# Performance work log

Measured on AMD Instinct MI355X. Metric: run time of the kernel, lower is better.

## Reference

```python
import jax, jax.numpy as jnp
import numpy as np

EPS = 1e-5  # BatchNorm eps

def gcn_conv(x, src, dst, deg, dinv, W, b):
    # PyG GCNConv: out = D^{-1/2}(A+I)D^{-1/2} X W + b
    N = x.shape[0]
    xw = x @ W                               # [N, F_out]
    norm = dinv[src] * dinv[dst]             # [E]
    agg = jax.ops.segment_sum(xw[src] * norm[:, None], dst, num_segments=N)
    agg = agg + xw * (1.0 / deg)[:, None]    # self-loop term: deg^-1/2 * deg^-1/2
    return agg + b

def bn(x, g, b, m, v):
    # inference-mode BatchNorm1d over features
    return (x - m) * jax.lax.rsqrt(v + EPS) * g + b

def setup_inputs() -> dict:
    key = jax.random.key(0)
    N, E, F_in, C = 100000, 1600000, 128, 16
    dims = [F_in, 64, 128, 64, 32, C]
    ks = jax.random.split(key, 64)
    inp = {}
    inp["x"] = jax.random.normal(ks[0], (N, F_in), dtype=jnp.float32)
    inp["edge_index"] = jax.random.randint(ks[1], (2, E), 0, N, dtype=jnp.int32)
    ki = 2
    for l in range(5):
        fi, fo = dims[l], dims[l + 1]
        scale = 1.0 / np.sqrt(fi)
        inp[f"w{l+1}"] = jax.random.normal(ks[ki], (fi, fo), dtype=jnp.float32) * scale; ki += 1
        inp[f"b{l+1}"] = jnp.zeros((fo,), dtype=jnp.float32)
    for l in range(4):  # BN params for layers 1..4
        fo = dims[l + 1]
        inp[f"g{l+1}"] = jnp.ones((fo,), dtype=jnp.float32)
        inp[f"be{l+1}"] = jnp.zeros((fo,), dtype=jnp.float32)
        inp[f"m{l+1}"] = jax.random.normal(ks[ki], (fo,), dtype=jnp.float32) * 0.1; ki += 1
        inp[f"v{l+1}"] = jax.random.uniform(ks[ki], (fo,), dtype=jnp.float32, minval=0.5, maxval=1.5); ki += 1
    return inp

def reference(x, edge_index,
              w1, b1, w2, b2, w3, b3, w4, b4, w5, b5,
              g1, be1, m1, v1, g2, be2, m2, v2,
              g3, be3, m3, v3, g4, be4, m4, v4):
    N = x.shape[0]
    src, dst = edge_index[0], edge_index[1]
    deg = jax.ops.segment_sum(jnp.ones(src.shape[0], x.dtype), dst, num_segments=N) + 1.0
    dinv = jax.lax.rsqrt(deg)
    h = jax.nn.relu(bn(gcn_conv(x, src, dst, deg, dinv, w1, b1), g1, be1, m1, v1))
    h = jax.nn.relu(bn(gcn_conv(h, src, dst, deg, dinv, w2, b2), g2, be2, m2, v2))
    h = jax.nn.relu(bn(gcn_conv(h, src, dst, deg, dinv, w3, b3), g3, be3, m3, v3))
    h = jax.nn.relu(bn(gcn_conv(h, src, dst, deg, dinv, w4, b4), g4, be4, m4, v4))
    return gcn_conv(h, src, dst, deg, dinv, w5, b5)
```

## Files before the change

kernel.cpp:

```cpp
#include <hip/hip_runtime.h>
#include <hip/hip_fp16.h>

#define BEPS 1e-5f
static constexpr int TPB = 256;
static constexpr int G_SC = 512;
static constexpr int BK_SHIFT = 8;
static constexpr int BK_NODES = 256;
static constexpr int KMAX = 512;
static constexpr int BK_SLACK = 2048;

union F4H8 { float4 f4; __half2 h2[4]; };

typedef _Float16 half8 __attribute__((ext_vector_type(8)));
typedef float floatx4 __attribute__((ext_vector_type(4)));


__global__ __launch_bounds__(TPB) void k_zero_int(int* __restrict__ p, int n) {
  int i = blockIdx.x * TPB + threadIdx.x;
  if (i < n) p[i] = 0;
}

__global__ __launch_bounds__(TPB) void k_hist(const int* __restrict__ dst,
                                              int* __restrict__ histG,
                                              int* __restrict__ btot,
                                              int E, int K, int chunk) {
  __shared__ int lh[KMAX];
  int g = blockIdx.x, t = threadIdx.x;
  for (int i = t; i < KMAX; i += TPB) lh[i] = 0;
  __syncthreads();
  int e0 = g * chunk, e1 = min(E, e0 + chunk);
  for (int e = e0 + t; e < e1; e += TPB) atomicAdd(&lh[dst[e] >> BK_SHIFT], 1);
  __syncthreads();
  for (int i = t; i < K; i += TPB) {
    histG[i * G_SC + g] = lh[i];
    atomicAdd(&btot[i], lh[i]);
  }
}

__global__ __launch_bounds__(KMAX) void k_bbase(const int* __restrict__ btot,
                                                int* __restrict__ bbase, int K) {
  __shared__ int sh[KMAX];
  int t = threadIdx.x;
  int v = (t < K) ? btot[t] : 0;
  sh[t] = v;
  __syncthreads();
  for (int s = 1; s < KMAX; s <<= 1) {
    int x = sh[t];
    int y = (t >= s) ? sh[t - s] : 0;
    __syncthreads();
    sh[t] = x + y;
    __syncthreads();
  }
  if (t < K) bbase[t] = sh[t] - v;
  if (t == 0) bbase[K] = sh[K - 1];
}

__global__ __launch_bounds__(G_SC) void k_offs(const int* __restrict__ histG,
                                               const int* __restrict__ bbase,
                                               int* __restrict__ offs) {
  __shared__ int sh[G_SC];
  int b = blockIdx.x, t = threadIdx.x;
  int v = histG[b * G_SC + t];
  sh[t] = v;
  __syncthreads();
  for (int s = 1; s < G_SC; s <<= 1) {
    int x = sh[t];
    int y = (t >= s) ? sh[t - s] : 0;
    __syncthreads();
    sh[t] = x + y;
    __syncthreads();
  }
  offs[b * G_SC + t] = bbase[b] + sh[t] - v;
}

__global__ __launch_bounds__(TPB) void k_scatter(const int* __restrict__ src,
                                                 const int* __restrict__ dst,
                                                 const int* __restrict__ offs,
                                                 unsigned int* __restrict__ pairs,
                                                 int E, int K, int chunk) {
  __shared__ int cur[KMAX];
  int g = blockIdx.x, t = threadIdx.x;
  for (int i = t; i < K; i += TPB) cur[i] = offs[i * G_SC + g];
  __syncthreads();
  int e0 = g * chunk, e1 = min(E, e0 + chunk);
  for (int e = e0 + t; e < e1; e += TPB) {
    int d = dst[e];
    int b = d >> BK_SHIFT;
    int pos = atomicAdd(&cur[b], 1);
    pairs[pos] = (unsigned int)src[e] | ((unsigned int)(d & (BK_NODES - 1)) << 20);
  }
}

__global__ __launch_bounds__(TPB) void k_bucket_sort(const unsigned int* __restrict__ pairs,
                                                     const int* __restrict__ bbase,
                                                     int* __restrict__ rowptr,
                                                     int* __restrict__ rowend,
                                                     int* __restrict__ colidx,
                                                     float* __restrict__ dinv,
                                                     int N, int E) {
  __shared__ int cur[BK_NODES];
  __shared__ int sh[BK_NODES];
  int b = blockIdx.x, t = threadIdx.x;
  int base = bbase[b], end = bbase[b + 1];
  int n0 = b << BK_SHIFT;
  int nNodes = min(BK_NODES, N - n0);
  cur[t] = 0;
  __syncthreads();
  for (int e = base + t; e < end; e += TPB) atomicAdd(&cur[pairs[e] >> 20], 1);
  __syncthreads();
  int v = cur[t];
  int pd = (v + 7) & ~7;
  sh[t] = pd;
  __syncthreads();
  for (int s = 1; s < TPB; s <<= 1) {
    int x = sh[t];
    int y = (t >= s) ? sh[t - s] : 0;
    __syncthreads();
    sh[t] = x + y;
    __syncthreads();
  }
  int Bb = (base + b * BK_SLACK + 7) & ~7;
  int start = Bb + (sh[t] - pd);
  if (t < nNodes) {
    rowptr[n0 + t] = start;
    rowend[n0 + t] = start + pd;
    dinv[n0 + t] = rsqrtf((float)(v + 1));
    for (int i = start + v; i < start + pd; ++i) colidx[i] = N;
  }
  __syncthreads();
  cur[t] = start;
  __syncthreads();
  for (int e = base + t; e < end; e += TPB) {
    unsigned int p = pairs[e];
    int pos = atomicAdd(&cur[p >> 20], 1);
    colidx[pos] = (int)(p & 0xFFFFFu);
  }
}

__device__ inline void packone(const float* __restrict__ W, _Float16* __restrict__ Wp,
                               int i, int FO) {
  int j = i & 7, lane = (i >> 3) & 63, tile = i >> 9;
  int nct = FO >> 4, ct = tile % nct, kch = tile / nct;
  int k = kch * 32 + ((lane >> 4) << 3) + j;
  int n = (ct << 4) + (lane & 15);
  Wp[i] = (_Float16)W[k * FO + n];
}

__global__ __launch_bounds__(TPB) void k_packAll(const float* w1, _Float16* p1,
                                                 const float* w2, _Float16* p2,
                                                 const float* w3, _Float16* p3,
                                                 const float* w4, _Float16* p4,
                                                 const float* w5, _Float16* p5,
                                                 __half* bufA, int N) {
  int i = blockIdx.x * TPB + threadIdx.x;
  if (i < 8192) packone(w1, p1, i, 64);
  else if (i < 16384) packone(w2, p2, i - 8192, 128);
  else if (i < 24576) packone(w3, p3, i - 16384, 64);
  else if (i < 26624) packone(w4, p4, i - 24576, 32);
  else if (i < 27136) packone(w5, p5, i - 26624, 16);
  else if (i < 27144) {
    float4 z = {0.f, 0.f, 0.f, 0.f};
    reinterpret_cast<float4*>(bufA + (size_t)64 * N)[i - 27136] = z;
  }
}

template <int FI, int FO, int EPI, bool F32IN>
__global__ __launch_bounds__(TPB) void k_mgemm(const void* __restrict__ hin,
                                               const _Float16* __restrict__ Wp,
                                               const float* __restrict__ dinv,
                                               const float* __restrict__ bias,
                                               const float* __restrict__ g,
                                               const float* __restrict__ be,
                                               const float* __restrict__ m,
                                               const float* __restrict__ v,
                                               __half* __restrict__ out, int N) {
  constexpr int NCT = FO / 16;
  constexpr int NKC = FI / 32;
  __shared__ float4 Wsh[NKC * NCT * 64];
  for (int i = threadIdx.x; i < NKC * NCT * 64; i += TPB)
    Wsh[i] = reinterpret_cast<const float4*>(Wp)[i];
  __syncthreads();

  int lane = threadIdx.x & 63;
  int wv = threadIdx.x >> 6;
  int quad = lane >> 4;
  int rowBase = blockIdx.x * 64 + wv * 16;
  int rA = min(rowBase + (lane & 15), N - 1);

  floatx4 acc[NCT];
#pragma unroll
  for (int ct = 0; ct < NCT; ++ct) acc[ct] = (floatx4){0.f, 0.f, 0.f, 0.f};

#pragma unroll
  for (int kch = 0; kch < NKC; ++kch) {
    half8 a;
    if constexpr (F32IN) {
      const float4* xp = reinterpret_cast<const float4*>(hin);
      size_t idx = ((size_t)rA * FI + kch * 32 + quad * 8) >> 2;
      float4 fa = xp[idx], fb = xp[idx + 1];
      a[0] = (_Float16)fa.x; a[1] = (_Float16)fa.y; a[2] = (_Float16)fa.z; a[3] = (_Float16)fa.w;
      a[4] = (_Float16)fb.x; a[5] = (_Float16)fb.y; a[6] = (_Float16)fb.z; a[7] = (_Float16)fb.w;
    } else {
      union { float4 f4; half8 h8; } ua;
      ua.f4 = reinterpret_cast<const float4*>(hin)[((size_t)rA * FI + kch * 32 + quad * 8) >> 3];
      a = ua.h8;
    }
#pragma unroll
    for (int ct = 0; ct < NCT; ++ct) {
      union { float4 f4; half8 h8; } ub;
      ub.f4 = Wsh[(kch * NCT + ct) * 64 + lane];
      acc[ct] = __builtin_amdgcn_mfma_f32_16x16x32_f16(a, ub.h8, acc[ct], 0, 0, 0);
    }
  }

  int r0 = rowBase + quad * 4;
  if (EPI == 0) {
    float dv[4];
#pragma unroll
    for (int reg = 0; reg < 4; ++reg) dv[reg] = (r0 + reg < N) ? dinv[r0 + reg] : 0.f;
#pragma unroll
    for (int ct = 0; ct < NCT; ++ct) {
      int col = ct * 16 + (lane & 15);
#pragma unroll
      for (int reg = 0; reg < 4; ++reg) {
        int r = r0 + reg;
        out[(size_t)r * FO + col] = __float2half(acc[ct][reg] * dv[reg]);
      }
    }
  } else {
#pragma unroll
    for (int ct = 0; ct < NCT; ++ct) {
      int col = ct * 16 + (lane & 15);
      float sc = g[col] * rsqrtf(v[col] + BEPS);
      float bb = bias[col] - m[col];
      float ee = be[col];
#pragma unroll
      for (int reg = 0; reg < 4; ++reg) {
        int r = r0 + reg;
        out[(size_t)r * FO + col] = __float2half(fmaxf((acc[ct][reg] + bb) * sc + ee, 0.f));
      }
    }
  }
}

template <int F, int MODE, typename TO>
__global__ __launch_bounds__(TPB) void k_agg(const __half* __restrict__ in,
                                             const int* __restrict__ rowptr,
                                             const int* __restrict__ rowend,
                                             const int* __restrict__ colidx,
                                             const float* __restrict__ dinv,
                                             const float* __restrict__ bias,
                                             const float* __restrict__ g,
                                             const float* __restrict__ be,
                                             const float* __restrict__ m,
                                             const float* __restrict__ v,
                                             TO* __restrict__ out, int N) {
  constexpr int V = F / 8;
  constexpr int NPB = TPB / V;
  int node = blockIdx.x * NPB + (int)(threadIdx.x / V);
  int lane = threadIdx.x % V;
  if (node >= N) return;
  const float4* in16 = reinterpret_cast<const float4*>(in);
  const size_t rs = F / 8;
  float acc[8];
  {
    F4H8 u;
    u.f4 = in16[(size_t)node * rs + lane];
#pragma unroll
    for (int i = 0; i < 4; ++i) {
      float2 t2 = __half22float2(u.h2[i]);
      acc[2 * i] = t2.x;
      acc[2 * i + 1] = t2.y;
    }
  }
  int e0 = rowptr[node], e1 = rowend[node];
  int4 c0, c1;
  if (e0 < e1) {
    c0 = *reinterpret_cast<const int4*>(colidx + e0);
    c1 = *reinterpret_cast<const int4*>(colidx + e0 + 4);
  }
  for (int e = e0; e < e1; e += 8) {
    int4 n0, n1;
    int en = e + 8;
    if (en < e1) {
      n0 = *reinterpret_cast<const int4*>(colidx + en);
      n1 = *reinterpret_cast<const int4*>(colidx + en + 4);
    }
    F4H8 u[8];
    u[0].f4 = in16[(size_t)c0.x * rs + lane];
    u[1].f4 = in16[(size_t)c0.y * rs + lane];
    u[2].f4 = in16[(size_t)c0.z * rs + lane];
    u[3].f4 = in16[(size_t)c0.w * rs + lane];
    u[4].f4 = in16[(size_t)c1.x * rs + lane];
    u[5].f4 = in16[(size_t)c1.y * rs + lane];
    u[6].f4 = in16[(size_t)c1.z * rs + lane];
    u[7].f4 = in16[(size_t)c1.w * rs + lane];
#pragma unroll
    for (int q = 0; q < 8; ++q) {
#pragma unroll
      for (int i = 0; i < 4; ++i) {
        float2 t2 = __half22float2(u[q].h2[i]);
        acc[2 * i] += t2.x;
        acc[2 * i + 1] += t2.y;
      }
    }
    c0 = n0; c1 = n1;
  }
  float dv = dinv[node];
#pragma unroll
  for (int i = 0; i < 8; ++i) acc[i] *= dv;
  if (MODE == 0) {
    float4 ba = reinterpret_cast<const float4*>(bias)[lane * 2];
    float4 bb = reinterpret_cast<const float4*>(bias)[lane * 2 + 1];
    acc[0] += ba.x; acc[1] += ba.y; acc[2] += ba.z; acc[3] += ba.w;
    acc[4] += bb.x; acc[5] += bb.y; acc[6] += bb.z; acc[7] += bb.w;
  } else if (MODE == 1 || MODE == 2) {
    const float4* B = reinterpret_cast<const float4*>(bias);
    const float4* G = reinterpret_cast<const float4*>(g);
    const float4* Be = reinterpret_cast<const float4*>(be);
    const float4* M = reinterpret_cast<const float4*>(m);
    const float4* Vv = reinterpret_cast<const float4*>(v);
#pragma unroll
    for (int h = 0; h < 2; ++h) {
      float4 b4 = B[lane * 2 + h], g4 = G[lane * 2 + h], e4 = Be[lane * 2 + h];
      float4 m4 = M[lane * 2 + h], v4 = Vv[lane * 2 + h];
      float* a = acc + 4 * h;
      a[0] = fmaxf((a[0] + b4.x - m4.x) * (g4.x * rsqrtf(v4.x + BEPS)) + e4.x, 0.f);
      a[1] = fmaxf((a[1] + b4.y - m4.y) * (g4.y * rsqrtf(v4.y + BEPS)) + e4.y, 0.f);
      a[2] = fmaxf((a[2] + b4.z - m4.z) * (g4.z * rsqrtf(v4.z + BEPS)) + e4.z, 0.f);
      a[3] = fmaxf((a[3] + b4.w - m4.w) * (g4.w * rsqrtf(v4.w + BEPS)) + e4.w, 0.f);
    }
    if (MODE == 2) {
#pragma unroll
      for (int i = 0; i < 8; ++i) acc[i] *= dv;
    }
  }
  if constexpr (sizeof(TO) == 2) {
    F4H8 u;
#pragma unroll
    for (int i = 0; i < 4; ++i) u.h2[i] = __floats2half2_rn(acc[2 * i], acc[2 * i + 1]);
    reinterpret_cast<float4*>(out)[(size_t)node * rs + lane] = u.f4;
  } else {
    float4 o0 = {acc[0], acc[1], acc[2], acc[3]};
    float4 o1 = {acc[4], acc[5], acc[6], acc[7]};
    float4* op = reinterpret_cast<float4*>((float*)out + (size_t)node * F + lane * 8);
    op[0] = o0;
    op[1] = o1;
  }
}


extern "C" void kernel_launch(void* const* d_in, const int* in_sizes, int n_in,
                              void* d_out, int out_size, void* d_ws, size_t ws_size,
                              hipStream_t stream) {
  const float* x = (const float*)d_in[0];
  const int* ei = (const int*)d_in[1];
  const int N = in_sizes[0] / 128;
  const int E = in_sizes[1] / 2;
  const int* src = ei;
  const int* dst = ei + E;

  const float* w1 = (const float*)d_in[2];  const float* b1 = (const float*)d_in[3];
  const float* w2 = (const float*)d_in[4];  const float* b2 = (const float*)d_in[5];
  const float* w3 = (const float*)d_in[6];  const float* b3 = (const float*)d_in[7];
  const float* w4 = (const float*)d_in[8];  const float* b4 = (const float*)d_in[9];
  const float* w5 = (const float*)d_in[10]; const float* b5 = (const float*)d_in[11];
  const float* g1 = (const float*)d_in[12]; const float* be1 = (const float*)d_in[13];
  const float* m1 = (const float*)d_in[14]; const float* v1 = (const float*)d_in[15];
  const float* g2 = (const float*)d_in[16]; const float* be2 = (const float*)d_in[17];
  const float* m2 = (const float*)d_in[18]; const float* v2 = (const float*)d_in[19];
  const float* g3 = (const float*)d_in[20]; const float* be3 = (const float*)d_in[21];
  const float* m3 = (const float*)d_in[22]; const float* v3 = (const float*)d_in[23];
  const float* g4 = (const float*)d_in[24]; const float* be4 = (const float*)d_in[25];
  const float* m4 = (const float*)d_in[26]; const float* v4 = (const float*)d_in[27];
  float* out = (float*)d_out;

  char* ws = (char*)d_ws;
  size_t off = 0;
  auto alloc = [&](size_t bytes) -> void* {
    void* p = ws + off;
    off += (bytes + 255) & ~(size_t)255;
    return p;
  };
  const int K = (N + BK_NODES - 1) >> BK_SHIFT;
  float*        dinv   = (float*)alloc((size_t)N * 4);
  int*          rowptr = (int*)alloc((size_t)N * 4);
  int*          rowend = (int*)alloc((size_t)N * 4);
  int*          colidx = (int*)alloc(((size_t)E + (size_t)(K + 1) * BK_SLACK) * 4);
  unsigned int* pairs  = (unsigned int*)alloc((size_t)E * 4);
  int*          histG  = (int*)alloc((size_t)KMAX * G_SC * 4);
  int*          offs   = (int*)alloc((size_t)KMAX * G_SC * 4);
  int*          btot   = (int*)alloc(KMAX * 4);
  int*          bbase  = (int*)alloc((KMAX + 1) * 4);
  _Float16*     wp1    = (_Float16*)alloc(128 * 64 * 2);
  _Float16*     wp2    = (_Float16*)alloc(64 * 128 * 2);
  _Float16*     wp3    = (_Float16*)alloc(128 * 64 * 2);
  _Float16*     wp4    = (_Float16*)alloc(64 * 32 * 2);
  _Float16*     wp5    = (_Float16*)alloc(32 * 16 * 2);
  __half*       bufA   = (__half*)alloc((size_t)(N + 64) * 128 * 2);
  __half*       bufB   = (__half*)alloc((size_t)(N + 64) * 128 * 2);
  (void)ws_size; (void)n_in; (void)out_size;

  const int chunk = (E + G_SC - 1) / G_SC;

  k_zero_int<<<2, TPB, 0, stream>>>(btot, KMAX);
  k_hist<<<G_SC, TPB, 0, stream>>>(dst, histG, btot, E, K, chunk);
  k_bbase<<<1, KMAX, 0, stream>>>(btot, bbase, K);
  k_offs<<<K, G_SC, 0, stream>>>(histG, bbase, offs);
  k_scatter<<<G_SC, TPB, 0, stream>>>(src, dst, offs, pairs, E, K, chunk);
  k_bucket_sort<<<K, TPB, 0, stream>>>(pairs, bbase, rowptr, rowend, colidx, dinv, N, E);

  k_packAll<<<(27144 + TPB - 1) / TPB, TPB, 0, stream>>>(w1, wp1, w2, wp2, w3, wp3, w4, wp4, w5, wp5, bufA, N);

  int gRow = (N + 63) / 64;
  k_mgemm<128, 64, 0, true><<<gRow, TPB, 0, stream>>>(x, wp1, dinv, nullptr, nullptr, nullptr, nullptr, nullptr, bufB, N);
  k_agg<64, 2, __half><<<(N + 31) / 32, TPB, 0, stream>>>(bufB, rowptr, rowend, colidx, dinv, b1, g1, be1, m1, v1, bufA, N);
  k_agg<64, 3, __half><<<(N + 31) / 32, TPB, 0, stream>>>(bufA, rowptr, rowend, colidx, dinv, nullptr, nullptr, nullptr, nullptr, nullptr, bufB, N);
  k_mgemm<64, 128, 1, false><<<gRow, TPB, 0, stream>>>(bufB, wp2, nullptr, b2, g2, be2, m2, v2, bufA, N);
  k_mgemm<128, 64, 0, false><<<gRow, TPB, 0, stream>>>(bufA, wp3, dinv, nullptr, nullptr, nullptr, nullptr, nullptr, bufB, N);
  k_agg<64, 1, __half><<<(N + 31) / 32, TPB, 0, stream>>>(bufB, rowptr, rowend, colidx, dinv, b3, g3, be3, m3, v3, bufA, N);
  k_mgemm<64, 32, 0, false><<<gRow, TPB, 0, stream>>>(bufA, wp4, dinv, nullptr, nullptr, nullptr, nullptr, nullptr, bufB, N);
  k_agg<32, 1, __half><<<(N + 63) / 64, TPB, 0, stream>>>(bufB, rowptr, rowend, colidx, dinv, b4, g4, be4, m4, v4, bufA, N);
  k_mgemm<32, 16, 0, false><<<gRow, TPB, 0, stream>>>(bufA, wp5, dinv, nullptr, nullptr, nullptr, nullptr, nullptr, bufB, N);
  k_agg<16, 0, float><<<(N + 127) / 128, TPB, 0, stream>>>(bufB, rowptr, rowend, colidx, dinv, b5, nullptr, nullptr, nullptr, nullptr, out, N);
}
```

Before: 363.8 us.

## Fuse layer-2 and layer-3 GEMMs via LDS and unroll aggregation gather to 16

```diff
diff --git a/kernel.cpp b/kernel.cpp
--- a/kernel.cpp
+++ b/kernel.cpp
@@ -239,6 +239,85 @@
         int r = r0 + reg;
         out[(size_t)r * FO + col] = __float2half(fmaxf((acc[ct][reg] + bb) * sc + ee, 0.f));
       }
+    }
+  }
+}
+
+__global__ __launch_bounds__(TPB) void k_mgemm23(const __half* __restrict__ hin,
+                                                 const _Float16* __restrict__ W2p,
+                                                 const _Float16* __restrict__ W3p,
+                                                 const float* __restrict__ dinv,
+                                                 const float* __restrict__ b2,
+                                                 const float* __restrict__ g2,
+                                                 const float* __restrict__ be2,
+                                                 const float* __restrict__ m2,
+                                                 const float* __restrict__ v2,
+                                                 __half* __restrict__ out, int N) {
+  __shared__ float4 W2s[2 * 8 * 64];
+  __shared__ float4 W3s[4 * 4 * 64];
+  __shared__ _Float16 tr[4 * 16 * 136];
+  for (int i = threadIdx.x; i < 1024; i += TPB) W2s[i] = reinterpret_cast<const float4*>(W2p)[i];
+  for (int i = threadIdx.x; i < 1024; i += TPB) W3s[i] = reinterpret_cast<const float4*>(W3p)[i];
+  __syncthreads();
+
+  int lane = threadIdx.x & 63;
+  int wv = threadIdx.x >> 6;
+  int quad = lane >> 4;
+  int m = lane & 15;
+  int rowBase = blockIdx.x * 64 + wv * 16;
+  int rA = min(rowBase + m, N - 1);
+
+  floatx4 acc1[8];
+#pragma unroll
+  for (int ct = 0; ct < 8; ++ct) acc1[ct] = (floatx4){0.f, 0.f, 0.f, 0.f};
+#pragma unroll
+  for (int kch = 0; kch < 2; ++kch) {
+    union { float4 f4; half8 h8; } ua;
+    ua.f4 = reinterpret_cast<const float4*>(hin)[((size_t)rA * 64 + kch * 32 + quad * 8) >> 3];
+#pragma unroll
+    for (int ct = 0; ct < 8; ++ct) {
+      union { float4 f4; half8 h8; } ub;
+      ub.f4 = W2s[(kch * 8 + ct) * 64 + lane];
+      acc1[ct] = __builtin_amdgcn_mfma_f32_16x16x32_f16(ua.h8, ub.h8, acc1[ct], 0, 0, 0);
+    }
+  }
+  _Float16* mytr = tr + wv * 16 * 136;
+#pragma unroll
+  for (int ct = 0; ct < 8; ++ct) {
+    int col = ct * 16 + m;
+    float sc = g2[col] * rsqrtf(v2[col] + BEPS);
+    float bb = b2[col] - m2[col];
+    float ee = be2[col];
+#pragma unroll
+    for (int reg = 0; reg < 4; ++reg) {
+      int r = quad * 4 + reg;
+      mytr[r * 136 + col] = (_Float16)fmaxf((acc1[ct][reg] + bb) * sc + ee, 0.f);
+    }
+  }
+  floatx4 acc2[4];
+#pragma unroll
+  for (int ct = 0; ct < 4; ++ct) acc2[ct] = (floatx4){0.f, 0.f, 0.f, 0.f};
+#pragma unroll
+  for (int kch = 0; kch < 4; ++kch) {
+    half8 a2 = *reinterpret_cast<const half8*>(&mytr[m * 136 + kch * 32 + quad * 8]);
+#pragma unroll
+    for (int ct = 0; ct < 4; ++ct) {
+      union { float4 f4; half8 h8; } ub;
+      ub.f4 = W3s[(kch * 4 + ct) * 64 + lane];
+      acc2[ct] = __builtin_amdgcn_mfma_f32_16x16x32_f16(a2, ub.h8, acc2[ct], 0, 0, 0);
+    }
+  }
+  int r0 = rowBase + quad * 4;
+  float dv[4];
+#pragma unroll
+  for (int reg = 0; reg < 4; ++reg) dv[reg] = (r0 + reg < N) ? dinv[r0 + reg] : 0.f;
+#pragma unroll
+  for (int ct = 0; ct < 4; ++ct) {
+    int col = ct * 16 + m;
+#pragma unroll
+    for (int reg = 0; reg < 4; ++reg) {
+      int r = r0 + reg;
+      out[(size_t)r * 64 + col] = __float2half(acc2[ct][reg] * dv[reg]);
     }
   }
 }
@@ -274,18 +353,42 @@
     }
   }
   int e0 = rowptr[node], e1 = rowend[node];
-  int4 c0, c1;
-  if (e0 < e1) {
-    c0 = *reinterpret_cast<const int4*>(colidx + e0);
-    c1 = *reinterpret_cast<const int4*>(colidx + e0 + 4);
-  }
-  for (int e = e0; e < e1; e += 8) {
-    int4 n0, n1;
-    int en = e + 8;
-    if (en < e1) {
-      n0 = *reinterpret_cast<const int4*>(colidx + en);
-      n1 = *reinterpret_cast<const int4*>(colidx + en + 4);
-    }
+  int e = e0;
+  for (; e + 16 <= e1; e += 16) {
+    int4 c0 = *reinterpret_cast<const int4*>(colidx + e);
+    int4 c1 = *reinterpret_cast<const int4*>(colidx + e + 4);
+    int4 c2 = *reinterpret_cast<const int4*>(colidx + e + 8);
+    int4 c3 = *reinterpret_cast<const int4*>(colidx + e + 12);
+    F4H8 u[16];
+    u[0].f4  = in16[(size_t)c0.x * rs + lane];
+    u[1].f4  = in16[(size_t)c0.y * rs + lane];
+    u[2].f4  = in16[(size_t)c0.z * rs + lane];
+    u[3].f4  = in16[(size_t)c0.w * rs + lane];
+    u[4].f4  = in16[(size_t)c1.x * rs + lane];
+    u[5].f4  = in16[(size_t)c1.y * rs + lane];
+    u[6].f4  = in16[(size_t)c1.z * rs + lane];
+    u[7].f4  = in16[(size_t)c1.w * rs + lane];
+    u[8].f4  = in16[(size_t)c2.x * rs + lane];
+    u[9].f4  = in16[(size_t)c2.y * rs + lane];
+    u[10].f4 = in16[(size_t)c2.z * rs + lane];
+    u[11].f4 = in16[(size_t)c2.w * rs + lane];
+    u[12].f4 = in16[(size_t)c3.x * rs + lane];
+    u[13].f4 = in16[(size_t)c3.y * rs + lane];
+    u[14].f4 = in16[(size_t)c3.z * rs + lane];
+    u[15].f4 = in16[(size_t)c3.w * rs + lane];
+#pragma unroll
+    for (int q = 0; q < 16; ++q) {
+#pragma unroll
+      for (int i = 0; i < 4; ++i) {
+        float2 t2 = __half22float2(u[q].h2[i]);
+        acc[2 * i] += t2.x;
+        acc[2 * i + 1] += t2.y;
+      }
+    }
+  }
+  if (e < e1) {
+    int4 c0 = *reinterpret_cast<const int4*>(colidx + e);
+    int4 c1 = *reinterpret_cast<const int4*>(colidx + e + 4);
     F4H8 u[8];
     u[0].f4 = in16[(size_t)c0.x * rs + lane];
     u[1].f4 = in16[(size_t)c0.y * rs + lane];
@@ -304,7 +407,6 @@
         acc[2 * i + 1] += t2.y;
       }
     }
-    c0 = n0; c1 = n1;
   }
   float dv = dinv[node];
 #pragma unroll
@@ -416,11 +518,10 @@
   k_mgemm<128, 64, 0, true><<<gRow, TPB, 0, stream>>>(x, wp1, dinv, nullptr, nullptr, nullptr, nullptr, nullptr, bufB, N);
   k_agg<64, 2, __half><<<(N + 31) / 32, TPB, 0, stream>>>(bufB, rowptr, rowend, colidx, dinv, b1, g1, be1, m1, v1, bufA, N);
   k_agg<64, 3, __half><<<(N + 31) / 32, TPB, 0, stream>>>(bufA, rowptr, rowend, colidx, dinv, nullptr, nullptr, nullptr, nullptr, nullptr, bufB, N);
-  k_mgemm<64, 128, 1, false><<<gRow, TPB, 0, stream>>>(bufB, wp2, nullptr, b2, g2, be2, m2, v2, bufA, N);
-  k_mgemm<128, 64, 0, false><<<gRow, TPB, 0, stream>>>(bufA, wp3, dinv, nullptr, nullptr, nullptr, nullptr, nullptr, bufB, N);
-  k_agg<64, 1, __half><<<(N + 31) / 32, TPB, 0, stream>>>(bufB, rowptr, rowend, colidx, dinv, b3, g3, be3, m3, v3, bufA, N);
-  k_mgemm<64, 32, 0, false><<<gRow, TPB, 0, stream>>>(bufA, wp4, dinv, nullptr, nullptr, nullptr, nullptr, nullptr, bufB, N);
-  k_agg<32, 1, __half><<<(N + 63) / 64, TPB, 0, stream>>>(bufB, rowptr, rowend, colidx, dinv, b4, g4, be4, m4, v4, bufA, N);
-  k_mgemm<32, 16, 0, false><<<gRow, TPB, 0, stream>>>(bufA, wp5, dinv, nullptr, nullptr, nullptr, nullptr, nullptr, bufB, N);
-  k_agg<16, 0, float><<<(N + 127) / 128, TPB, 0, stream>>>(bufB, rowptr, rowend, colidx, dinv, b5, nullptr, nullptr, nullptr, nullptr, out, N);
-}
+  k_mgemm23<<<gRow, TPB, 0, stream>>>(bufB, wp2, wp3, dinv, b2, g2, be2, m2, v2, bufA, N);
+  k_agg<64, 1, __half><<<(N + 31) / 32, TPB, 0, stream>>>(bufA, rowptr, rowend, colidx, dinv, b3, g3, be3, m3, v3, bufB, N);
+  k_mgemm<64, 32, 0, false><<<gRow, TPB, 0, stream>>>(bufB, wp4, dinv, nullptr, nullptr, nullptr, nullptr, nullptr, bufA, N);
+  k_agg<32, 1, __half><<<(N + 63) / 64, TPB, 0, stream>>>(bufA, rowptr, rowend, colidx, dinv, b4, g4, be4, m4, v4, bufB, N);
+  k_mgemm<32, 16, 0, false><<<gRow, TPB, 0, stream>>>(bufB, wp5, dinv, nullptr, nullptr, nullptr, nullptr, nullptr, bufA, N);
+  k_agg<16, 0, float><<<(N + 127) / 128, TPB, 0, stream>>>(bufA, rowptr, rowend, colidx, dinv, b5, nullptr, nullptr, nullptr, nullptr, out, N);
+}
```

Measured after the change: 360.4 us. No clear change (-0.9%).
